# Kernel optimization log

Hardware: AMD Instinct MI355X
Metric: run time of the kernel (lower is better)

## Reference

```python
import jax, jax.numpy as jnp
import numpy as np
from jax import lax

DIM = 256
HEAD_DIM = 64          # v head dim and hedgehog dim
HEAD_DIM_QK = 64       # must equal HEAD_DIM for the module to run
NH = DIM // HEAD_DIM   # 4
EPS = 1e-6


def setup_inputs() -> dict:
    key = jax.random.key(0)
    ks = jax.random.split(key, 12)
    B, C, H, W, D = 1, DIM, 16, 16, 16
    x = jax.random.normal(ks[0], (B, C, H, W, D), dtype=jnp.float32)
    qk_dim = HEAD_DIM_QK * NH
    # 1x1x1 conv weights for q, k (qkv_bias=False)
    Wq = jax.random.normal(ks[1], (qk_dim, C), dtype=jnp.float32) * 0.02
    Wk = jax.random.normal(ks[2], (qk_dim, C), dtype=jnp.float32) * 0.02
    # depthwise 3x3x3 conv for v (groups=dim, bias=True)
    Wv = jax.random.normal(ks[3], (C, 1, 3, 3, 3), dtype=jnp.float32) * 0.1
    bv = jax.random.normal(ks[4], (C,), dtype=jnp.float32) * 0.02
    # HedgeHog linear layers (init is identity/zeros; use near-identity + noise)
    eye = jnp.eye(HEAD_DIM, dtype=jnp.float32)
    Wmq = eye * 0.5 + jax.random.normal(ks[5], (HEAD_DIM, HEAD_DIM), dtype=jnp.float32) * 0.02
    bmq = jnp.zeros((HEAD_DIM,), dtype=jnp.float32)
    Wmk = eye * 0.5 + jax.random.normal(ks[6], (HEAD_DIM, HEAD_DIM), dtype=jnp.float32) * 0.02
    bmk = jnp.zeros((HEAD_DIM,), dtype=jnp.float32)
    Wmv = eye * 0.5 + jax.random.normal(ks[7], (HEAD_DIM, HEAD_DIM), dtype=jnp.float32) * 0.02
    bmv = jnp.zeros((HEAD_DIM,), dtype=jnp.float32)
    return {"x": x, "Wq": Wq, "Wk": Wk, "Wv": Wv, "bv": bv,
            "Wmq": Wmq, "bmq": bmq, "Wmk": Wmk, "bmk": bmk,
            "Wmv": Wmv, "bmv": bmv}


def _hedgehog(z, W, b):
    # z: [B, nh, N, d] -> [B, 2*nh, N, d]; cat along HEAD axis (dim=1) as in torch code
    h = jnp.einsum('bhnd,ed->bhne', z, W) + b
    return jnp.concatenate([jnp.exp(h), jnp.exp(-h)], axis=1)


def reference(x, Wq, Wk, Wv, bv, Wmq, bmq, Wmk, bmk, Wmv, bmv):
    B, C, H, W_, D = x.shape
    N = H * W_ * D
    x2 = x.reshape(B, C, N)
    # 1x1x1 conv projections
    q = jnp.einsum('oc,bcn->bon', Wq, x2)  # [B, qk_dim, N]
    k = jnp.einsum('oc,bcn->bon', Wk, x2)
    # depthwise 3x3x3 conv for v
    v3 = lax.conv_general_dilated(
        x, Wv, window_strides=(1, 1, 1),
        padding=((1, 1), (1, 1), (1, 1)),
        dimension_numbers=('NCDHW', 'OIDHW', 'NCDHW'),
        feature_group_count=C) + bv[None, :, None, None, None]
    v = v3.reshape(B, C, N)
    # split heads, tokens-last -> tokens axis
    q1 = q.reshape(B, NH, HEAD_DIM_QK, N).transpose(0, 1, 3, 2)  # [B,nh,N,dqk]
    k1 = k.reshape(B, NH, HEAD_DIM_QK, N).transpose(0, 1, 3, 2)
    v1 = v.reshape(B, NH, HEAD_DIM, N).transpose(0, 1, 3, 2)     # [B,nh,N,dv]
    qf = _hedgehog(q1, Wmq, bmq)  # [B,2nh,N,dqk]
    kf = _hedgehog(k1, Wmk, bmk)
    vf = _hedgehog(v1, Wmv, bmv)  # [B,2nh,N,dv]
    # quadratic "linear" attention: row-sum normalized QK^T
    qk = jnp.einsum('bhmd,bhnd->bhmn', qf, kf)          # [B,2nh,N,N]
    attn = qk / (jnp.sum(qk, axis=-1, keepdims=True) + EPS)
    out = jnp.einsum('bhmn,bhnd->bhmd', attn, vf)        # [B,2nh,N,dv]
    out = out.transpose(0, 1, 3, 2).reshape(B, 2 * C, H, W_, D)
    return out
```

## Files before the change

### kernel.cpp

```cpp
#include <hip/hip_runtime.h>
#include <math.h>

#define EPS_F 1e-6f

typedef __attribute__((ext_vector_type(8))) short bf16x8;
typedef __attribute__((ext_vector_type(4))) float f32x4;

#define OFF_BV  0
#define OFF_VC  (OFF_BV + 256)
#define OFF_PS  (OFF_VC + 256*4096)
#define OFF_PSV (OFF_PS + 8*64*4096)
#define OFF_SM  (OFF_PSV + 8*64*64)
#define OFF_SV  (OFF_SM + 8*4096)
#define OFF_QF  (OFF_SV + 512)
#define OFF_WQH (OFF_QF + 512*4096)
#define OFF_WQL (OFF_WQH + 32768)
#define OFF_WKH (OFF_WQL + 32768)
#define OFF_WKL (OFF_WKH + 32768)
#define OFF_XTH (OFF_WKL + 32768)
#define OFF_XTL (OFF_XTH + 524288)

__device__ __forceinline__ void split_bf16(float v, unsigned short& h, unsigned short& l) {
    unsigned int b = __float_as_uint(v);
    h = (unsigned short)(b >> 16);
    float fh = __uint_as_float(b & 0xFFFF0000u);
    l = (unsigned short)(__float_as_uint(v - fh) >> 16);
}

__global__ __launch_bounds__(256) void k_combine(
    const float* __restrict__ Wq, const float* __restrict__ Wk,
    const float* __restrict__ Wmq, const float* __restrict__ Wmk,
    const float* __restrict__ Wmv, const float* __restrict__ bmv,
    const float* __restrict__ bv, float* __restrict__ ws)
{
    int row = blockIdx.x;
    int c = threadIdx.x;
    int h = row >> 6, e = row & 63;
    float aq = 0.f, ak = 0.f;
    for (int d = 0; d < 64; ++d) {
        float mq = Wmq[e*64 + d];
        float mk = Wmk[e*64 + d];
        int src = (h*64 + d)*256 + c;
        aq = fmaf(mq, Wq[src], aq);
        ak = fmaf(mk, Wk[src], ak);
    }
    unsigned short hh, ll;
    unsigned short* WQH = (unsigned short*)(ws + OFF_WQH);
    unsigned short* WQL = (unsigned short*)(ws + OFF_WQL);
    unsigned short* WKH = (unsigned short*)(ws + OFF_WKH);
    unsigned short* WKL = (unsigned short*)(ws + OFF_WKL);
    split_bf16(aq, hh, ll); WQH[row*256 + c] = hh; WQL[row*256 + c] = ll;
    split_bf16(ak, hh, ll); WKH[row*256 + c] = hh; WKL[row*256 + c] = ll;
    if (c == 0) {
        float av = 0.f;
        for (int d = 0; d < 64; ++d) av = fmaf(Wmv[e*64 + d], bv[h*64 + d], av);
        ws[OFF_BV + row] = av + bmv[e];
    }
}

__global__ __launch_bounds__(256) void k_xt(
    const float* __restrict__ x, float* __restrict__ ws)
{
    __shared__ float Ts[64][65];
    int tx = blockIdx.x;
    int cy = blockIdx.y;
    int t = threadIdx.x;
    int lr = t >> 6, lc2 = t & 63;
    #pragma unroll
    for (int i = 0; i < 16; ++i) {
        int row = lr*16 + i;
        Ts[row][lc2] = x[(size_t)(cy*64 + row)*4096 + tx*64 + lc2];
    }
    __syncthreads();
    int tok = t >> 2, c16 = (t & 3) * 16;
    unsigned int hw[8], lw[8];
    #pragma unroll
    for (int j = 0; j < 8; ++j) {
        float v0 = Ts[c16 + 2*j][tok], v1 = Ts[c16 + 2*j + 1][tok];
        unsigned int b0 = __float_as_uint(v0), b1 = __float_as_uint(v1);
        hw[j] = (b0 >> 16) | (b1 & 0xFFFF0000u);
        float f0 = __uint_as_float(b0 & 0xFFFF0000u);
        float f1 = __uint_as_float(b1 & 0xFFFF0000u);
        lw[j] = (__float_as_uint(v0 - f0) >> 16) | (__float_as_uint(v1 - f1) & 0xFFFF0000u);
    }
    unsigned short* XH = (unsigned short*)(ws + OFF_XTH);
    unsigned short* XL = (unsigned short*)(ws + OFF_XTL);
    size_t base = (size_t)(tx*64 + tok)*256 + cy*64 + c16;
    uint4 H0 = {hw[0], hw[1], hw[2], hw[3]}, H1 = {hw[4], hw[5], hw[6], hw[7]};
    uint4 L0 = {lw[0], lw[1], lw[2], lw[3]}, L1 = {lw[4], lw[5], lw[6], lw[7]};
    *(uint4*)(XH + base) = H0;  *(uint4*)(XH + base + 8) = H1;
    *(uint4*)(XL + base) = L0;  *(uint4*)(XL + base + 8) = L1;
}

__global__ __launch_bounds__(256) void k_dwconv(
    const float* __restrict__ x, const float* __restrict__ Wv, float* __restrict__ vc)
{
    int c = blockIdx.y;
    int n = blockIdx.x * 256 + threadIdx.x;
    int z = n >> 8, y = (n >> 4) & 15, xx = n & 15;
    const float* xc = x + c * 4096;
    const float* wc = Wv + c * 27;
    float acc = 0.f;
    #pragma unroll
    for (int kz = 0; kz < 3; ++kz) {
        int zz = z + kz - 1;
        if (zz < 0 || zz > 15) continue;
        #pragma unroll
        for (int ky = 0; ky < 3; ++ky) {
            int yy = y + ky - 1;
            if (yy < 0 || yy > 15) continue;
            #pragma unroll
            for (int kx = 0; kx < 3; ++kx) {
                int xv = xx + kx - 1;
                if (xv < 0 || xv > 15) continue;
                acc = fmaf(wc[(kz*3 + ky)*3 + kx], xc[(zz << 8) + (yy << 4) + xv], acc);
            }
        }
    }
    vc[c*4096 + n] = acc;
}

__global__ __launch_bounds__(512, 2) void k_fused(
    const float* __restrict__ bmk, const float* __restrict__ bmq,
    const float* __restrict__ Wmv, float* __restrict__ ws)
{
    __shared__ float smem[16384];
    unsigned short* su = (unsigned short*)smem;

    int t = threadIdx.x;
    int chunk = blockIdx.x;
    int hb = blockIdx.y;
    int n0 = chunk * 64;
    int w = t >> 6, lane = t & 63;
    int kq = w >> 2;
    int mh = w & 1, nh = (w >> 1) & 1;
    int l15 = lane & 15, l4 = lane >> 4;
    bool isQ = (t >= 256);
    int tl = t & 255;
    int lc = tl >> 6, ln = tl & 63;
    int e4 = (tl & 15) * 4;
    int n4 = (tl >> 4) * 4;

    const unsigned short* XH  = (const unsigned short*)(ws + OFF_XTH);
    const unsigned short* XL  = (const unsigned short*)(ws + OFF_XTL);
    const unsigned short* WKHp = (const unsigned short*)(ws + OFF_WKH);
    const unsigned short* WKLp = (const unsigned short*)(ws + OFF_WKL);
    const unsigned short* WQHp = (const unsigned short*)(ws + OFF_WQH);
    const unsigned short* WQLp = (const unsigned short*)(ws + OFF_WQL);

    f32x4 acc[2][2];
    #pragma unroll
    for (int i = 0; i < 2; ++i)
        #pragma unroll
        for (int j = 0; j < 2; ++j) acc[i][j] = (f32x4){0.f, 0.f, 0.f, 0.f};
    float accV[4][4];
    #pragma unroll
    for (int i = 0; i < 4; ++i)
        #pragma unroll
        for (int j = 0; j < 4; ++j) accV[i][j] = 0.f;

    for (int cs = 0; cs < 4; ++cs) {
        int c0 = cs * 64;
        {
            int r = (t >> 3) & 63, s = t & 7;
            unsigned short* d = su + r*64 + (((s ^ (r & 7))) << 3);
            size_t xo = (size_t)(n0 + r)*256 + c0 + s*8;
            size_t wo = (size_t)(hb*64 + r)*256 + c0 + s*8;
            *(uint4*)(d)         = *(const uint4*)(XH + xo);
            *(uint4*)(d + 4096)  = *(const uint4*)(XL + xo);
            *(uint4*)(d + 8192)  = *(const uint4*)(WKHp + wo);
            *(uint4*)(d + 12288) = *(const uint4*)(WKLp + wo);
            *(uint4*)(d + 16384) = *(const uint4*)(WQHp + wo);
            *(uint4*)(d + 20480) = *(const uint4*)(WQLp + wo);
        }
        __syncthreads();
        const unsigned short* Xh = su;
        const unsigned short* Xl = su + 4096;
        const unsigned short* Wh = su + 8192 + kq*8192;
        const unsigned short* Wl = Wh + 4096;
        #pragma unroll
        for (int ks = 0; ks < 2; ++ks) {
            bf16x8 ah[2], al[2], bh_[2], bl_[2];
            #pragma unroll
            for (int mt = 0; mt < 2; ++mt) {
                int ar = mh*32 + mt*16 + l15;
                int off = ar*64 + (((ks*4 + l4) ^ (ar & 7)) << 3);
                ah[mt] = *(const bf16x8*)(Xh + off);
                al[mt] = *(const bf16x8*)(Xl + off);
            }
            #pragma unroll
            for (int nt = 0; nt < 2; ++nt) {
                int br = nh*32 + nt*16 + l15;
                int off = br*64 + (((ks*4 + l4) ^ (br & 7)) << 3);
                bh_[nt] = *(const bf16x8*)(Wh + off);
                bl_[nt] = *(const bf16x8*)(Wl + off);
            }
            #pragma unroll
            for (int mt = 0; mt < 2; ++mt)
                #pragma unroll
                for (int nt = 0; nt < 2; ++nt) {
                    acc[mt][nt] = __builtin_amdgcn_mfma_f32_16x16x32_bf16(ah[mt], bh_[nt], acc[mt][nt], 0, 0, 0);
                    acc[mt][nt] = __builtin_amdgcn_mfma_f32_16x16x32_bf16(al[mt], bh_[nt], acc[mt][nt], 0, 0, 0);
                    acc[mt][nt] = __builtin_amdgcn_mfma_f32_16x16x32_bf16(ah[mt], bl_[nt], acc[mt][nt], 0, 0, 0);
                }
        }
        __syncthreads();
    }

    float (*Xs)[64]  = (float(*)[64])smem;
    float (*Wsh)[68] = (float(*)[68])(smem + 4096);
    if (!isQ) {
        const float* vcb = ws + OFF_VC + (size_t)hb*64*4096;
        #pragma unroll
        for (int i = 0; i < 16; ++i)
            Xs[lc*16 + i][ln] = vcb[(size_t)(lc*16 + i)*4096 + n0 + ln];
        #pragma unroll
        for (int i = 0; i < 16; ++i) { int idx = i*256 + tl; Wsh[idx & 63][idx >> 6] = Wmv[idx]; }
    }
    __syncthreads();

    if (!isQ) {
        #pragma unroll 4
        for (int d = 0; d < 64; ++d) {
            float4 xv4 = *(const float4*)&Xs[d][n4];
            float4 wv4 = *(const float4*)&Wsh[d][e4];
            float xv[4] = {xv4.x, xv4.y, xv4.z, xv4.w};
            float wv[4] = {wv4.x, wv4.y, wv4.z, wv4.w};
            #pragma unroll
            for (int ii = 0; ii < 4; ++ii)
                #pragma unroll
                for (int jj = 0; jj < 4; ++jj)
                    accV[ii][jj] = fmaf(xv[ii], wv[jj], accV[ii][jj]);
        }
    }
    __syncthreads();

    float (*kfp)[64] = (float(*)[64])smem;
    float (*kfm)[64] = (float(*)[64])(smem + 4096);
    float (*vfp)[64] = (float(*)[64])(smem + 8192);
    float (*vfm)[64] = (float(*)[64])(smem + 12288);
    if (!isQ) {
        float bk0 = bmk[nh*32 + l15], bk1 = bmk[nh*32 + 16 + l15];
        #pragma unroll
        for (int mt = 0; mt < 2; ++mt)
            #pragma unroll
            for (int nt = 0; nt < 2; ++nt) {
                float bkv = nt ? bk1 : bk0;
                int feat = nh*32 + nt*16 + l15;
                #pragma unroll
                for (int r = 0; r < 4; ++r) {
                    int tok = mh*32 + mt*16 + l4*4 + r;
                    float v = acc[mt][nt][r] + bkv;
                    kfp[tok][feat] = __expf(v);
                    kfm[tok][feat] = __expf(-v);
                }
            }
        float bvv[4];
        #pragma unroll
        for (int j = 0; j < 4; ++j) bvv[j] = ws[OFF_BV + hb*64 + e4 + j];
        #pragma unroll
        for (int ii = 0; ii < 4; ++ii) {
            float pv[4], mv[4];
            #pragma unroll
            for (int jj = 0; jj < 4; ++jj) {
                float b = accV[ii][jj] + bvv[jj];
                pv[jj] = __expf(b);  mv[jj] = __expf(-b);
            }
            *(float4*)&vfp[n4 + ii][e4] = make_float4(pv[0], pv[1], pv[2], pv[3]);
            *(float4*)&vfm[n4 + ii][e4] = make_float4(mv[0], mv[1], mv[2], mv[3]);
        }
    }
    __syncthreads();

    float aSp[4][4], aSm[4][4], svp[4], svm[4];
    #pragma unroll
    for (int i = 0; i < 4; ++i) {
        svp[i] = 0.f; svm[i] = 0.f;
        #pragma unroll
        for (int j = 0; j < 4; ++j) { aSp[i][j] = 0.f; aSm[i][j] = 0.f; }
    }
    int a4 = e4, f4 = n4;
    int nb = isQ ? 32 : 0;
    #pragma unroll 2
    for (int nn = 0; nn < 32; ++nn) {
        int n = nb + nn;
        float4 kp4 = *(const float4*)&kfp[n][a4];
        float4 km4 = *(const float4*)&kfm[n][a4];
        float4 vp4 = *(const float4*)&vfp[n][f4];
        float4 vm4 = *(const float4*)&vfm[n][f4];
        float kp[4] = {kp4.x, kp4.y, kp4.z, kp4.w};
        float km[4] = {km4.x, km4.y, km4.z, km4.w};
        float vp[4] = {vp4.x, vp4.y, vp4.z, vp4.w};
        float vm[4] = {vm4.x, vm4.y, vm4.z, vm4.w};
        #pragma unroll
        for (int ai = 0; ai < 4; ++ai) {
            svp[ai] += kp[ai];  svm[ai] += km[ai];
            #pragma unroll
            for (int fi = 0; fi < 4; ++fi) {
                aSp[ai][fi] = fmaf(kp[ai], vp[fi], aSp[ai][fi]);
                aSm[ai][fi] = fmaf(km[ai], vm[fi], aSm[ai][fi]);
            }
        }
    }
    __syncthreads();

    if (isQ) {
        #pragma unroll
        for (int i = 0; i < 4; ++i)
            #pragma unroll
            for (int j = 0; j < 4; ++j) {
                smem[(i*4 + j)*256 + tl]      = aSp[i][j];
                smem[(16 + i*4 + j)*256 + tl] = aSm[i][j];
            }
        if (tl < 16) {
            #pragma unroll
            for (int i = 0; i < 4; ++i) {
                smem[8192 + i*16 + tl]      = svp[i];
                smem[8192 + 64 + i*16 + tl] = svm[i];
            }
        }
    }
    __syncthreads();
    if (!isQ) {
        #pragma unroll
        for (int i = 0; i < 4; ++i)
            #pragma unroll
            for (int j = 0; j < 4; ++j) {
                aSp[i][j] += smem[(i*4 + j)*256 + tl];
                aSm[i][j] += smem[(16 + i*4 + j)*256 + tl];
            }
        float* pSp = ws + OFF_PS + (size_t)(hb*64 + chunk)*4096;
        float* pSm = ws + OFF_PS + (size_t)((hb + 4)*64 + chunk)*4096;
        #pragma unroll
        for (int ai = 0; ai < 4; ++ai) {
            *(float4*)&pSp[(a4 + ai)*64 + f4] = make_float4(aSp[ai][0], aSp[ai][1], aSp[ai][2], aSp[ai][3]);
            *(float4*)&pSm[(a4 + ai)*64 + f4] = make_float4(aSm[ai][0], aSm[ai][1], aSm[ai][2], aSm[ai][3]);
        }
        if (tl < 16) {
            #pragma unroll
            for (int i = 0; i < 4; ++i) {
                svp[i] += smem[8192 + i*16 + tl];
                svm[i] += smem[8192 + 64 + i*16 + tl];
            }
            float* pvp = ws + OFF_PSV + (size_t)(hb*64 + chunk)*64;
            float* pvm = ws + OFF_PSV + (size_t)((hb + 4)*64 + chunk)*64;
            *(float4*)&pvp[a4] = make_float4(svp[0], svp[1], svp[2], svp[3]);
            *(float4*)&pvm[a4] = make_float4(svm[0], svm[1], svm[2], svm[3]);
        }
    }
    __syncthreads();

    float (*qTp)[68] = (float(*)[68])smem;
    float (*qTm)[68] = (float(*)[68])(smem + 4352);
    if (isQ) {
        float bq0 = bmq[nh*32 + l15], bq1 = bmq[nh*32 + 16 + l15];
        #pragma unroll
        for (int mt = 0; mt < 2; ++mt)
            #pragma unroll
            for (int nt = 0; nt < 2; ++nt) {
                float bqv = nt ? bq1 : bq0;
                int feat = nh*32 + nt*16 + l15;
                #pragma unroll
                for (int r = 0; r < 4; ++r) {
                    int tok = mh*32 + mt*16 + l4*4 + r;
                    float v = acc[mt][nt][r] + bqv;
                    qTp[feat][tok] = __expf(v);
                    qTm[feat][tok] = __expf(-v);
                }
            }
    }
    __syncthreads();
    float* gq = ws + OFF_QF;
    #pragma unroll
    for (int j = 0; j < 4; ++j) {
        int un = t + 512*j;
        int s = un >> 10;
        int rem = un & 1023;
        int feat = rem >> 4, t4 = (rem & 15) * 4;
        const float* src = (s ? &qTm[feat][t4] : &qTp[feat][t4]);
        float4 v = *(const float4*)src;
        *(float4*)&gq[(size_t)((hb + 4*s)*64 + feat)*4096 + n0 + t4] = v;
    }
}

__global__ __launch_bounds__(256) void k_reduce(float* __restrict__ ws)
{
    int idx = blockIdx.x*256 + threadIdx.x;
    if (idx < 8*4096) {
        int h = idx >> 12, r = idx & 4095;
        float s = 0.f;
        #pragma unroll 16
        for (int c = 0; c < 64; ++c) s += ws[OFF_PS + (size_t)(h*64 + c)*4096 + r];
        ws[OFF_SM + idx] = s;
    } else if (idx < 8*4096 + 512) {
        int j = idx - 8*4096;
        int h = j >> 6, e = j & 63;
        float s = 0.f;
        #pragma unroll 16
        for (int c = 0; c < 64; ++c) s += ws[OFF_PSV + (size_t)(h*64 + c)*64 + e];
        ws[OFF_SV + j] = s;
    }
}

__global__ __launch_bounds__(256, 2) void k_out(
    const float* __restrict__ ws, float* __restrict__ out)
{
    __shared__ float qs[64][64];
    __shared__ float Sms[64][64];
    __shared__ float svs[64];
    int t = threadIdx.x;
    int chunk = blockIdx.x;
    int h = blockIdx.y;
    int n0 = chunk * 64;
    int lc = t >> 6, ln = t & 63;

    const float* gq = ws + OFF_QF + (size_t)h*64*4096;
    #pragma unroll
    for (int i = 0; i < 16; ++i)
        qs[lc*16 + i][ln] = gq[(size_t)(lc*16 + i)*4096 + n0 + ln];
    const float* Smg = ws + OFF_SM + (size_t)h*4096;
    #pragma unroll
    for (int i = 0; i < 16; ++i) { int idx = i*256 + t; Sms[idx >> 6][idx & 63] = Smg[idx]; }
    if (t < 64) svs[t] = ws[OFF_SV + h*64 + t];
    __syncthreads();

    int n4 = (t & 15) * 4;
    int e4 = (t >> 4) * 4;
    float acc[4][4];
    float den[4] = {0.f, 0.f, 0.f, 0.f};
    #pragma unroll
    for (int i = 0; i < 4; ++i)
        #pragma unroll
        for (int j = 0; j < 4; ++j) acc[i][j] = 0.f;
    #pragma unroll 4
    for (int a = 0; a < 64; ++a) {
        float4 qv4 = *(const float4*)&qs[a][n4];
        float4 sm4 = *(const float4*)&Sms[a][e4];
        float qv[4] = {qv4.x, qv4.y, qv4.z, qv4.w};
        float sm[4] = {sm4.x, sm4.y, sm4.z, sm4.w};
        float sva = svs[a];
        #pragma unroll
        for (int nj = 0; nj < 4; ++nj) {
            den[nj] = fmaf(qv[nj], sva, den[nj]);
            #pragma unroll
            for (int ei = 0; ei < 4; ++ei)
                acc[ei][nj] = fmaf(sm[ei], qv[nj], acc[ei][nj]);
        }
    }
    float r[4];
    #pragma unroll
    for (int nj = 0; nj < 4; ++nj) r[nj] = 1.f / (den[nj] + EPS_F);
    #pragma unroll
    for (int ei = 0; ei < 4; ++ei)
        *(float4*)&out[(size_t)(h*64 + e4 + ei)*4096 + n0 + n4] =
            make_float4(acc[ei][0]*r[0], acc[ei][1]*r[1], acc[ei][2]*r[2], acc[ei][3]*r[3]);
}

extern "C" void kernel_launch(void* const* d_in, const int* in_sizes, int n_in,
                              void* d_out, int out_size, void* d_ws, size_t ws_size,
                              hipStream_t stream) {
    const float* x   = (const float*)d_in[0];
    const float* Wq  = (const float*)d_in[1];
    const float* Wk  = (const float*)d_in[2];
    const float* Wv  = (const float*)d_in[3];
    const float* bv  = (const float*)d_in[4];
    const float* Wmq = (const float*)d_in[5];
    const float* bmq = (const float*)d_in[6];
    const float* Wmk = (const float*)d_in[7];
    const float* bmk = (const float*)d_in[8];
    const float* Wmv = (const float*)d_in[9];
    const float* bmv = (const float*)d_in[10];
    float* out = (float*)d_out;
    float* ws  = (float*)d_ws;

    k_combine<<<256, 256, 0, stream>>>(Wq, Wk, Wmq, Wmk, Wmv, bmv, bv, ws);
    k_xt<<<dim3(64, 4), 256, 0, stream>>>(x, ws);
    k_dwconv<<<dim3(16, 256), 256, 0, stream>>>(x, Wv, ws + OFF_VC);
    k_fused<<<dim3(64, 4), 512, 0, stream>>>(bmk, bmq, Wmv, ws);
    k_reduce<<<130, 256, 0, stream>>>(ws);
    k_out<<<dim3(64, 8), 256, 0, stream>>>(ws, out);
}
```

Measured before the change: 133.2 us.

## Merge six kernels into one cooperative persistent kernel with grid syncs

Replaces the six separate launches (weight combine, x transpose/split, depthwise conv, fused projection, reduce, output) with a single cooperative kernel of 256 blocks of 512 threads. The stages are separated by grid.sync() barriers, and each block's work is remapped onto its block index. This removes per-launch overhead and inter-kernel gaps for a small, latency-bound problem. In exchange it adds grid-wide barrier cost, and some stages such as the reduce and output run with fewer or idle threads per block.

```diff
diff --git a/kernel.cpp b/kernel.cpp
--- a/kernel.cpp
+++ b/kernel.cpp
@@ -1,5 +1,8 @@
 #include <hip/hip_runtime.h>
+#include <hip/hip_cooperative_groups.h>
 #include <math.h>
+
+namespace cg = cooperative_groups;
 
 #define EPS_F 1e-6f
 
@@ -27,433 +30,436 @@
     l = (unsigned short)(__float_as_uint(v - fh) >> 16);
 }
 
-__global__ __launch_bounds__(256) void k_combine(
+__global__ __launch_bounds__(512, 2) void k_mega(
+    const float* __restrict__ x,
     const float* __restrict__ Wq, const float* __restrict__ Wk,
-    const float* __restrict__ Wmq, const float* __restrict__ Wmk,
+    const float* __restrict__ Wv, const float* __restrict__ bv,
+    const float* __restrict__ Wmq, const float* __restrict__ bmq,
+    const float* __restrict__ Wmk, const float* __restrict__ bmk,
     const float* __restrict__ Wmv, const float* __restrict__ bmv,
-    const float* __restrict__ bv, float* __restrict__ ws)
-{
-    int row = blockIdx.x;
-    int c = threadIdx.x;
-    int h = row >> 6, e = row & 63;
-    float aq = 0.f, ak = 0.f;
-    for (int d = 0; d < 64; ++d) {
-        float mq = Wmq[e*64 + d];
-        float mk = Wmk[e*64 + d];
-        int src = (h*64 + d)*256 + c;
-        aq = fmaf(mq, Wq[src], aq);
-        ak = fmaf(mk, Wk[src], ak);
-    }
-    unsigned short hh, ll;
-    unsigned short* WQH = (unsigned short*)(ws + OFF_WQH);
-    unsigned short* WQL = (unsigned short*)(ws + OFF_WQL);
-    unsigned short* WKH = (unsigned short*)(ws + OFF_WKH);
-    unsigned short* WKL = (unsigned short*)(ws + OFF_WKL);
-    split_bf16(aq, hh, ll); WQH[row*256 + c] = hh; WQL[row*256 + c] = ll;
-    split_bf16(ak, hh, ll); WKH[row*256 + c] = hh; WKL[row*256 + c] = ll;
-    if (c == 0) {
-        float av = 0.f;
-        for (int d = 0; d < 64; ++d) av = fmaf(Wmv[e*64 + d], bv[h*64 + d], av);
-        ws[OFF_BV + row] = av + bmv[e];
-    }
-}
-
-__global__ __launch_bounds__(256) void k_xt(
-    const float* __restrict__ x, float* __restrict__ ws)
-{
-    __shared__ float Ts[64][65];
-    int tx = blockIdx.x;
-    int cy = blockIdx.y;
-    int t = threadIdx.x;
-    int lr = t >> 6, lc2 = t & 63;
-    #pragma unroll
-    for (int i = 0; i < 16; ++i) {
-        int row = lr*16 + i;
-        Ts[row][lc2] = x[(size_t)(cy*64 + row)*4096 + tx*64 + lc2];
-    }
-    __syncthreads();
-    int tok = t >> 2, c16 = (t & 3) * 16;
-    unsigned int hw[8], lw[8];
-    #pragma unroll
-    for (int j = 0; j < 8; ++j) {
-        float v0 = Ts[c16 + 2*j][tok], v1 = Ts[c16 + 2*j + 1][tok];
-        unsigned int b0 = __float_as_uint(v0), b1 = __float_as_uint(v1);
-        hw[j] = (b0 >> 16) | (b1 & 0xFFFF0000u);
-        float f0 = __uint_as_float(b0 & 0xFFFF0000u);
-        float f1 = __uint_as_float(b1 & 0xFFFF0000u);
-        lw[j] = (__float_as_uint(v0 - f0) >> 16) | (__float_as_uint(v1 - f1) & 0xFFFF0000u);
-    }
-    unsigned short* XH = (unsigned short*)(ws + OFF_XTH);
-    unsigned short* XL = (unsigned short*)(ws + OFF_XTL);
-    size_t base = (size_t)(tx*64 + tok)*256 + cy*64 + c16;
-    uint4 H0 = {hw[0], hw[1], hw[2], hw[3]}, H1 = {hw[4], hw[5], hw[6], hw[7]};
-    uint4 L0 = {lw[0], lw[1], lw[2], lw[3]}, L1 = {lw[4], lw[5], lw[6], lw[7]};
-    *(uint4*)(XH + base) = H0;  *(uint4*)(XH + base + 8) = H1;
-    *(uint4*)(XL + base) = L0;  *(uint4*)(XL + base + 8) = L1;
-}
-
-__global__ __launch_bounds__(256) void k_dwconv(
-    const float* __restrict__ x, const float* __restrict__ Wv, float* __restrict__ vc)
-{
-    int c = blockIdx.y;
-    int n = blockIdx.x * 256 + threadIdx.x;
-    int z = n >> 8, y = (n >> 4) & 15, xx = n & 15;
-    const float* xc = x + c * 4096;
-    const float* wc = Wv + c * 27;
-    float acc = 0.f;
-    #pragma unroll
-    for (int kz = 0; kz < 3; ++kz) {
-        int zz = z + kz - 1;
-        if (zz < 0 || zz > 15) continue;
-        #pragma unroll
-        for (int ky = 0; ky < 3; ++ky) {
-            int yy = y + ky - 1;
-            if (yy < 0 || yy > 15) continue;
-            #pragma unroll
-            for (int kx = 0; kx < 3; ++kx) {
-                int xv = xx + kx - 1;
-                if (xv < 0 || xv > 15) continue;
-                acc = fmaf(wc[(kz*3 + ky)*3 + kx], xc[(zz << 8) + (yy << 4) + xv], acc);
-            }
-        }
-    }
-    vc[c*4096 + n] = acc;
-}
-
-__global__ __launch_bounds__(512, 2) void k_fused(
-    const float* __restrict__ bmk, const float* __restrict__ bmq,
-    const float* __restrict__ Wmv, float* __restrict__ ws)
+    float* __restrict__ ws, float* __restrict__ out)
 {
     __shared__ float smem[16384];
-    unsigned short* su = (unsigned short*)smem;
-
+    cg::grid_group grid = cg::this_grid();
+    int b = blockIdx.x;
     int t = threadIdx.x;
-    int chunk = blockIdx.x;
-    int hb = blockIdx.y;
-    int n0 = chunk * 64;
-    int w = t >> 6, lane = t & 63;
-    int kq = w >> 2;
-    int mh = w & 1, nh = (w >> 1) & 1;
-    int l15 = lane & 15, l4 = lane >> 4;
-    bool isQ = (t >= 256);
-    int tl = t & 255;
-    int lc = tl >> 6, ln = tl & 63;
-    int e4 = (tl & 15) * 4;
-    int n4 = (tl >> 4) * 4;
-
-    const unsigned short* XH  = (const unsigned short*)(ws + OFF_XTH);
-    const unsigned short* XL  = (const unsigned short*)(ws + OFF_XTL);
-    const unsigned short* WKHp = (const unsigned short*)(ws + OFF_WKH);
-    const unsigned short* WKLp = (const unsigned short*)(ws + OFF_WKL);
-    const unsigned short* WQHp = (const unsigned short*)(ws + OFF_WQH);
-    const unsigned short* WQLp = (const unsigned short*)(ws + OFF_WQL);
-
-    f32x4 acc[2][2];
-    #pragma unroll
-    for (int i = 0; i < 2; ++i)
-        #pragma unroll
-        for (int j = 0; j < 2; ++j) acc[i][j] = (f32x4){0.f, 0.f, 0.f, 0.f};
-    float accV[4][4];
-    #pragma unroll
-    for (int i = 0; i < 4; ++i)
-        #pragma unroll
-        for (int j = 0; j < 4; ++j) accV[i][j] = 0.f;
-
-    for (int cs = 0; cs < 4; ++cs) {
-        int c0 = cs * 64;
-        {
-            int r = (t >> 3) & 63, s = t & 7;
-            unsigned short* d = su + r*64 + (((s ^ (r & 7))) << 3);
-            size_t xo = (size_t)(n0 + r)*256 + c0 + s*8;
-            size_t wo = (size_t)(hb*64 + r)*256 + c0 + s*8;
-            *(uint4*)(d)         = *(const uint4*)(XH + xo);
-            *(uint4*)(d + 4096)  = *(const uint4*)(XL + xo);
-            *(uint4*)(d + 8192)  = *(const uint4*)(WKHp + wo);
-            *(uint4*)(d + 12288) = *(const uint4*)(WKLp + wo);
-            *(uint4*)(d + 16384) = *(const uint4*)(WQHp + wo);
-            *(uint4*)(d + 20480) = *(const uint4*)(WQLp + wo);
-        }
-        __syncthreads();
-        const unsigned short* Xh = su;
-        const unsigned short* Xl = su + 4096;
-        const unsigned short* Wh = su + 8192 + kq*8192;
-        const unsigned short* Wl = Wh + 4096;
-        #pragma unroll
-        for (int ks = 0; ks < 2; ++ks) {
-            bf16x8 ah[2], al[2], bh_[2], bl_[2];
-            #pragma unroll
-            for (int mt = 0; mt < 2; ++mt) {
-                int ar = mh*32 + mt*16 + l15;
-                int off = ar*64 + (((ks*4 + l4) ^ (ar & 7)) << 3);
-                ah[mt] = *(const bf16x8*)(Xh + off);
-                al[mt] = *(const bf16x8*)(Xl + off);
-            }
-            #pragma unroll
-            for (int nt = 0; nt < 2; ++nt) {
-                int br = nh*32 + nt*16 + l15;
-                int off = br*64 + (((ks*4 + l4) ^ (br & 7)) << 3);
-                bh_[nt] = *(const bf16x8*)(Wh + off);
-                bl_[nt] = *(const bf16x8*)(Wl + off);
-            }
+
+    if (t < 256) {
+        int row = b, c = t;
+        int h = row >> 6, e = row & 63;
+        float aq = 0.f, ak = 0.f;
+        for (int d = 0; d < 64; ++d) {
+            float mq = Wmq[e*64 + d];
+            float mk = Wmk[e*64 + d];
+            int src = (h*64 + d)*256 + c;
+            aq = fmaf(mq, Wq[src], aq);
+            ak = fmaf(mk, Wk[src], ak);
+        }
+        unsigned short hh, ll;
+        unsigned short* WQH = (unsigned short*)(ws + OFF_WQH);
+        unsigned short* WQL = (unsigned short*)(ws + OFF_WQL);
+        unsigned short* WKH = (unsigned short*)(ws + OFF_WKH);
+        unsigned short* WKL = (unsigned short*)(ws + OFF_WKL);
+        split_bf16(aq, hh, ll); WQH[row*256 + c] = hh; WQL[row*256 + c] = ll;
+        split_bf16(ak, hh, ll); WKH[row*256 + c] = hh; WKL[row*256 + c] = ll;
+        if (c == 0) {
+            float av = 0.f;
+            for (int d = 0; d < 64; ++d) av = fmaf(Wmv[e*64 + d], bv[h*64 + d], av);
+            ws[OFF_BV + row] = av + bmv[e];
+        }
+    }
+    {
+        float (*Ts)[65] = (float(*)[65])smem;
+        int tx = b & 63, cy = b >> 6;
+        int lr = t >> 6, lc2 = t & 63;
+        #pragma unroll
+        for (int i = 0; i < 8; ++i) {
+            int row = lr*8 + i;
+            Ts[row][lc2] = x[(size_t)(cy*64 + row)*4096 + tx*64 + lc2];
+        }
+        __syncthreads();
+        int tok = t >> 3, c8 = (t & 7) * 8;
+        unsigned int hw[4], lw[4];
+        #pragma unroll
+        for (int j = 0; j < 4; ++j) {
+            float v0 = Ts[c8 + 2*j][tok], v1 = Ts[c8 + 2*j + 1][tok];
+            unsigned int b0 = __float_as_uint(v0), b1 = __float_as_uint(v1);
+            hw[j] = (b0 >> 16) | (b1 & 0xFFFF0000u);
+            float f0 = __uint_as_float(b0 & 0xFFFF0000u);
+            float f1 = __uint_as_float(b1 & 0xFFFF0000u);
+            lw[j] = (__float_as_uint(v0 - f0) >> 16) | (__float_as_uint(v1 - f1) & 0xFFFF0000u);
+        }
+        unsigned short* XH = (unsigned short*)(ws + OFF_XTH);
+        unsigned short* XL = (unsigned short*)(ws + OFF_XTL);
+        size_t base = (size_t)(tx*64 + tok)*256 + cy*64 + c8;
+        uint4 H = {hw[0], hw[1], hw[2], hw[3]};
+        uint4 L = {lw[0], lw[1], lw[2], lw[3]};
+        *(uint4*)(XH + base) = H;
+        *(uint4*)(XL + base) = L;
+        __syncthreads();
+    }
+    {
+        int c = b;
+        const float* xc = x + c * 4096;
+        const float* wc = Wv + c * 27;
+        #pragma unroll
+        for (int i = 0; i < 8; ++i) {
+            int n = t + 512*i;
+            int z = n >> 8, y = (n >> 4) & 15, xx = n & 15;
+            float acc = 0.f;
+            #pragma unroll
+            for (int kz = 0; kz < 3; ++kz) {
+                int zz = z + kz - 1;
+                if (zz < 0 || zz > 15) continue;
+                #pragma unroll
+                for (int ky = 0; ky < 3; ++ky) {
+                    int yy = y + ky - 1;
+                    if (yy < 0 || yy > 15) continue;
+                    #pragma unroll
+                    for (int kx = 0; kx < 3; ++kx) {
+                        int xv = xx + kx - 1;
+                        if (xv < 0 || xv > 15) continue;
+                        acc = fmaf(wc[(kz*3 + ky)*3 + kx], xc[(zz << 8) + (yy << 4) + xv], acc);
+                    }
+                }
+            }
+            ws[OFF_VC + (size_t)c*4096 + n] = acc;
+        }
+    }
+    grid.sync();
+
+    {
+        unsigned short* su = (unsigned short*)smem;
+        int chunk = b & 63;
+        int hb = b >> 6;
+        int n0 = chunk * 64;
+        int w = t >> 6, lane = t & 63;
+        int kq = w >> 2;
+        int mh = w & 1, nh = (w >> 1) & 1;
+        int l15 = lane & 15, l4 = lane >> 4;
+        bool isQ = (t >= 256);
+        int tl = t & 255;
+        int lc = tl >> 6, ln = tl & 63;
+        int e4 = (tl & 15) * 4;
+        int n4 = (tl >> 4) * 4;
+
+        const unsigned short* XH  = (const unsigned short*)(ws + OFF_XTH);
+        const unsigned short* XL  = (const unsigned short*)(ws + OFF_XTL);
+        const unsigned short* WKHp = (const unsigned short*)(ws + OFF_WKH);
+        const unsigned short* WKLp = (const unsigned short*)(ws + OFF_WKL);
+        const unsigned short* WQHp = (const unsigned short*)(ws + OFF_WQH);
+        const unsigned short* WQLp = (const unsigned short*)(ws + OFF_WQL);
+
+        f32x4 acc[2][2];
+        #pragma unroll
+        for (int i = 0; i < 2; ++i)
+            #pragma unroll
+            for (int j = 0; j < 2; ++j) acc[i][j] = (f32x4){0.f, 0.f, 0.f, 0.f};
+        float accV[4][4];
+        #pragma unroll
+        for (int i = 0; i < 4; ++i)
+            #pragma unroll
+            for (int j = 0; j < 4; ++j) accV[i][j] = 0.f;
+
+        for (int cs = 0; cs < 4; ++cs) {
+            int c0 = cs * 64;
+            {
+                int r = (t >> 3) & 63, s = t & 7;
+                unsigned short* d = su + r*64 + (((s ^ (r & 7))) << 3);
+                size_t xo = (size_t)(n0 + r)*256 + c0 + s*8;
+                size_t wo = (size_t)(hb*64 + r)*256 + c0 + s*8;
+                *(uint4*)(d)         = *(const uint4*)(XH + xo);
+                *(uint4*)(d + 4096)  = *(const uint4*)(XL + xo);
+                *(uint4*)(d + 8192)  = *(const uint4*)(WKHp + wo);
+                *(uint4*)(d + 12288) = *(const uint4*)(WKLp + wo);
+                *(uint4*)(d + 16384) = *(const uint4*)(WQHp + wo);
+                *(uint4*)(d + 20480) = *(const uint4*)(WQLp + wo);
+            }
+            __syncthreads();
+            const unsigned short* Xh = su;
+            const unsigned short* Xl = su + 4096;
+            const unsigned short* Wh = su + 8192 + kq*8192;
+            const unsigned short* Wl = Wh + 4096;
+            #pragma unroll
+            for (int ks = 0; ks < 2; ++ks) {
+                bf16x8 ah[2], al[2], bh_[2], bl_[2];
+                #pragma unroll
+                for (int mt = 0; mt < 2; ++mt) {
+                    int ar = mh*32 + mt*16 + l15;
+                    int off = ar*64 + (((ks*4 + l4) ^ (ar & 7)) << 3);
+                    ah[mt] = *(const bf16x8*)(Xh + off);
+                    al[mt] = *(const bf16x8*)(Xl + off);
+                }
+                #pragma unroll
+                for (int nt = 0; nt < 2; ++nt) {
+                    int br = nh*32 + nt*16 + l15;
+                    int off = br*64 + (((ks*4 + l4) ^ (br & 7)) << 3);
+                    bh_[nt] = *(const bf16x8*)(Wh + off);
+                    bl_[nt] = *(const bf16x8*)(Wl + off);
+                }
+                #pragma unroll
+                for (int mt = 0; mt < 2; ++mt)
+                    #pragma unroll
+                    for (int nt = 0; nt < 2; ++nt) {
+                        acc[mt][nt] = __builtin_amdgcn_mfma_f32_16x16x32_bf16(ah[mt], bh_[nt], acc[mt][nt], 0, 0, 0);
+                        acc[mt][nt] = __builtin_amdgcn_mfma_f32_16x16x32_bf16(al[mt], bh_[nt], acc[mt][nt], 0, 0, 0);
+                        acc[mt][nt] = __builtin_amdgcn_mfma_f32_16x16x32_bf16(ah[mt], bl_[nt], acc[mt][nt], 0, 0, 0);
+                    }
+            }
+            __syncthreads();
+        }
+
+        float (*Xs)[64]  = (float(*)[64])smem;
+        float (*Wsh)[68] = (float(*)[68])(smem + 4096);
+        if (!isQ) {
+            const float* vcb = ws + OFF_VC + (size_t)hb*64*4096;
+            #pragma unroll
+            for (int i = 0; i < 16; ++i)
+                Xs[lc*16 + i][ln] = vcb[(size_t)(lc*16 + i)*4096 + n0 + ln];
+            #pragma unroll
+            for (int i = 0; i < 16; ++i) { int idx = i*256 + tl; Wsh[idx & 63][idx >> 6] = Wmv[idx]; }
+        }
+        __syncthreads();
+
+        if (!isQ) {
+            #pragma unroll 4
+            for (int d = 0; d < 64; ++d) {
+                float4 xv4 = *(const float4*)&Xs[d][n4];
+                float4 wv4 = *(const float4*)&Wsh[d][e4];
+                float xv[4] = {xv4.x, xv4.y, xv4.z, xv4.w};
+                float wv[4] = {wv4.x, wv4.y, wv4.z, wv4.w};
+                #pragma unroll
+                for (int ii = 0; ii < 4; ++ii)
+                    #pragma unroll
+                    for (int jj = 0; jj < 4; ++jj)
+                        accV[ii][jj] = fmaf(xv[ii], wv[jj], accV[ii][jj]);
+            }
+        }
+        __syncthreads();
+
+        float (*kfp)[64] = (float(*)[64])smem;
+        float (*kfm)[64] = (float(*)[64])(smem + 4096);
+        float (*vfp)[64] = (float(*)[64])(smem + 8192);
+        float (*vfm)[64] = (float(*)[64])(smem + 12288);
+        if (!isQ) {
+            float bk0 = bmk[nh*32 + l15], bk1 = bmk[nh*32 + 16 + l15];
             #pragma unroll
             for (int mt = 0; mt < 2; ++mt)
                 #pragma unroll
                 for (int nt = 0; nt < 2; ++nt) {
-                    acc[mt][nt] = __builtin_amdgcn_mfma_f32_16x16x32_bf16(ah[mt], bh_[nt], acc[mt][nt], 0, 0, 0);
-                    acc[mt][nt] = __builtin_amdgcn_mfma_f32_16x16x32_bf16(al[mt], bh_[nt], acc[mt][nt], 0, 0, 0);
-                    acc[mt][nt] = __builtin_amdgcn_mfma_f32_16x16x32_bf16(ah[mt], bl_[nt], acc[mt][nt], 0, 0, 0);
-                }
-        }
-        __syncthreads();
-    }
-
-    float (*Xs)[64]  = (float(*)[64])smem;
-    float (*Wsh)[68] = (float(*)[68])(smem + 4096);
-    if (!isQ) {
-        const float* vcb = ws + OFF_VC + (size_t)hb*64*4096;
+                    float bkv = nt ? bk1 : bk0;
+                    int feat = nh*32 + nt*16 + l15;
+                    #pragma unroll
+                    for (int r = 0; r < 4; ++r) {
+                        int tok = mh*32 + mt*16 + l4*4 + r;
+                        float v = acc[mt][nt][r] + bkv;
+                        kfp[tok][feat] = __expf(v);
+                        kfm[tok][feat] = __expf(-v);
+                    }
+                }
+            float bvv[4];
+            #pragma unroll
+            for (int j = 0; j < 4; ++j) bvv[j] = ws[OFF_BV + hb*64 + e4 + j];
+            #pragma unroll
+            for (int ii = 0; ii < 4; ++ii) {
+                float pv[4], mv[4];
+                #pragma unroll
+                for (int jj = 0; jj < 4; ++jj) {
+                    float bb = accV[ii][jj] + bvv[jj];
+                    pv[jj] = __expf(bb);  mv[jj] = __expf(-bb);
+                }
+                *(float4*)&vfp[n4 + ii][e4] = make_float4(pv[0], pv[1], pv[2], pv[3]);
+                *(float4*)&vfm[n4 + ii][e4] = make_float4(mv[0], mv[1], mv[2], mv[3]);
+            }
+        }
+        __syncthreads();
+
+        float aSp[4][4], aSm[4][4], svp[4], svm[4];
+        #pragma unroll
+        for (int i = 0; i < 4; ++i) {
+            svp[i] = 0.f; svm[i] = 0.f;
+            #pragma unroll
+            for (int j = 0; j < 4; ++j) { aSp[i][j] = 0.f; aSm[i][j] = 0.f; }
+        }
+        int a4 = e4, f4 = n4;
+        int nb = isQ ? 32 : 0;
+        #pragma unroll 2
+        for (int nn = 0; nn < 32; ++nn) {
+            int n = nb + nn;
+            float4 kp4 = *(const float4*)&kfp[n][a4];
+            float4 km4 = *(const float4*)&kfm[n][a4];
+            float4 vp4 = *(const float4*)&vfp[n][f4];
+            float4 vm4 = *(const float4*)&vfm[n][f4];
+            float kp[4] = {kp4.x, kp4.y, kp4.z, kp4.w};
+            float km[4] = {km4.x, km4.y, km4.z, km4.w};
+            float vp[4] = {vp4.x, vp4.y, vp4.z, vp4.w};
+            float vm[4] = {vm4.x, vm4.y, vm4.z, vm4.w};
+            #pragma unroll
+            for (int ai = 0; ai < 4; ++ai) {
+                svp[ai] += kp[ai];  svm[ai] += km[ai];
+                #pragma unroll
+                for (int fi = 0; fi < 4; ++fi) {
+                    aSp[ai][fi] = fmaf(kp[ai], vp[fi], aSp[ai][fi]);
+                    aSm[ai][fi] = fmaf(km[ai], vm[fi], aSm[ai][fi]);
+                }
+            }
+        }
+        __syncthreads();
+
+        if (isQ) {
+            #pragma unroll
+            for (int i = 0; i < 4; ++i)
+                #pragma unroll
+                for (int j = 0; j < 4; ++j) {
+                    smem[(i*4 + j)*256 + tl]      = aSp[i][j];
+                    smem[(16 + i*4 + j)*256 + tl] = aSm[i][j];
+                }
+            if (tl < 16) {
+                #pragma unroll
+                for (int i = 0; i < 4; ++i) {
+                    smem[8192 + i*16 + tl]      = svp[i];
+                    smem[8192 + 64 + i*16 + tl] = svm[i];
+                }
+            }
+        }
+        __syncthreads();
+        if (!isQ) {
+            #pragma unroll
+            for (int i = 0; i < 4; ++i)
+                #pragma unroll
+                for (int j = 0; j < 4; ++j) {
+                    aSp[i][j] += smem[(i*4 + j)*256 + tl];
+                    aSm[i][j] += smem[(16 + i*4 + j)*256 + tl];
+                }
+            float* pSp = ws + OFF_PS + (size_t)(hb*64 + chunk)*4096;
+            float* pSm = ws + OFF_PS + (size_t)((hb + 4)*64 + chunk)*4096;
+            #pragma unroll
+            for (int ai = 0; ai < 4; ++ai) {
+                *(float4*)&pSp[(a4 + ai)*64 + f4] = make_float4(aSp[ai][0], aSp[ai][1], aSp[ai][2], aSp[ai][3]);
+                *(float4*)&pSm[(a4 + ai)*64 + f4] = make_float4(aSm[ai][0], aSm[ai][1], aSm[ai][2], aSm[ai][3]);
+            }
+            if (tl < 16) {
+                #pragma unroll
+                for (int i = 0; i < 4; ++i) {
+                    svp[i] += smem[8192 + i*16 + tl];
+                    svm[i] += smem[8192 + 64 + i*16 + tl];
+                }
+                float* pvp = ws + OFF_PSV + (size_t)(hb*64 + chunk)*64;
+                float* pvm = ws + OFF_PSV + (size_t)((hb + 4)*64 + chunk)*64;
+                *(float4*)&pvp[a4] = make_float4(svp[0], svp[1], svp[2], svp[3]);
+                *(float4*)&pvm[a4] = make_float4(svm[0], svm[1], svm[2], svm[3]);
+            }
+        }
+        __syncthreads();
+
+        float (*qTp)[68] = (float(*)[68])smem;
+        float (*qTm)[68] = (float(*)[68])(smem + 4352);
+        if (isQ) {
+            float bq0 = bmq[nh*32 + l15], bq1 = bmq[nh*32 + 16 + l15];
+            #pragma unroll
+            for (int mt = 0; mt < 2; ++mt)
+                #pragma unroll
+                for (int nt = 0; nt < 2; ++nt) {
+                    float bqv = nt ? bq1 : bq0;
+                    int feat = nh*32 + nt*16 + l15;
+                    #pragma unroll
+                    for (int r = 0; r < 4; ++r) {
+                        int tok = mh*32 + mt*16 + l4*4 + r;
+                        float v = acc[mt][nt][r] + bqv;
+                        qTp[feat][tok] = __expf(v);
+                        qTm[feat][tok] = __expf(-v);
+                    }
+                }
+        }
+        __syncthreads();
+        float* gq = ws + OFF_QF;
+        #pragma unroll
+        for (int j = 0; j < 4; ++j) {
+            int un = t + 512*j;
+            int s = un >> 10;
+            int rem = un & 1023;
+            int feat = rem >> 4, t4 = (rem & 15) * 4;
+            const float* src = (s ? &qTm[feat][t4] : &qTp[feat][t4]);
+            float4 v = *(const float4*)src;
+            *(float4*)&gq[(size_t)((hb + 4*s)*64 + feat)*4096 + n0 + t4] = v;
+        }
+    }
+    grid.sync();
+
+    {
+        int idx = b*512 + t;
+        if (idx < 8*4096) {
+            int h = idx >> 12, r = idx & 4095;
+            float s = 0.f;
+            #pragma unroll 16
+            for (int c = 0; c < 64; ++c) s += ws[OFF_PS + (size_t)(h*64 + c)*4096 + r];
+            ws[OFF_SM + idx] = s;
+        } else if (idx < 8*4096 + 512) {
+            int j = idx - 8*4096;
+            int h = j >> 6, e = j & 63;
+            float s = 0.f;
+            #pragma unroll 16
+            for (int c = 0; c < 64; ++c) s += ws[OFF_PSV + (size_t)(h*64 + c)*64 + e];
+            ws[OFF_SV + j] = s;
+        }
+    }
+    grid.sync();
+
+    {
+        float* qs0 = smem;
+        float* qs1 = smem + 4096;
+        float (*Sms)[64] = (float(*)[64])(smem + 8192);
+        float* svs = smem + 12288;
+        int h = b >> 5;
+        int uh = t >> 8, th = t & 255;
+        int chunk = (b & 31) * 2 + uh;
+        int n0 = chunk * 64;
+        float* qs = uh ? qs1 : qs0;
+        int lc = th >> 6, ln = th & 63;
+
+        const float* gq = ws + OFF_QF + (size_t)h*64*4096;
         #pragma unroll
         for (int i = 0; i < 16; ++i)
-            Xs[lc*16 + i][ln] = vcb[(size_t)(lc*16 + i)*4096 + n0 + ln];
-        #pragma unroll
-        for (int i = 0; i < 16; ++i) { int idx = i*256 + tl; Wsh[idx & 63][idx >> 6] = Wmv[idx]; }
-    }
-    __syncthreads();
-
-    if (!isQ) {
+            qs[(lc*16 + i)*64 + ln] = gq[(size_t)(lc*16 + i)*4096 + n0 + ln];
+        if (uh == 0) {
+            const float* Smg = ws + OFF_SM + (size_t)h*4096;
+            #pragma unroll
+            for (int i = 0; i < 16; ++i) { int idx = i*256 + th; Sms[idx >> 6][idx & 63] = Smg[idx]; }
+        }
+        if (t < 64) svs[t] = ws[OFF_SV + h*64 + t];
+        __syncthreads();
+
+        int n4 = (th & 15) * 4;
+        int e4 = (th >> 4) * 4;
+        float acc[4][4];
+        float den[4] = {0.f, 0.f, 0.f, 0.f};
+        #pragma unroll
+        for (int i = 0; i < 4; ++i)
+            #pragma unroll
+            for (int j = 0; j < 4; ++j) acc[i][j] = 0.f;
         #pragma unroll 4
-        for (int d = 0; d < 64; ++d) {
-            float4 xv4 = *(const float4*)&Xs[d][n4];
-            float4 wv4 = *(const float4*)&Wsh[d][e4];
-            float xv[4] = {xv4.x, xv4.y, xv4.z, xv4.w};
-            float wv[4] = {wv4.x, wv4.y, wv4.z, wv4.w};
-            #pragma unroll
-            for (int ii = 0; ii < 4; ++ii)
-                #pragma unroll
-                for (int jj = 0; jj < 4; ++jj)
-                    accV[ii][jj] = fmaf(xv[ii], wv[jj], accV[ii][jj]);
-        }
-    }
-    __syncthreads();
-
-    float (*kfp)[64] = (float(*)[64])smem;
-    float (*kfm)[64] = (float(*)[64])(smem + 4096);
-    float (*vfp)[64] = (float(*)[64])(smem + 8192);
-    float (*vfm)[64] = (float(*)[64])(smem + 12288);
-    if (!isQ) {
-        float bk0 = bmk[nh*32 + l15], bk1 = bmk[nh*32 + 16 + l15];
-        #pragma unroll
-        for (int mt = 0; mt < 2; ++mt)
-            #pragma unroll
-            for (int nt = 0; nt < 2; ++nt) {
-                float bkv = nt ? bk1 : bk0;
-                int feat = nh*32 + nt*16 + l15;
-                #pragma unroll
-                for (int r = 0; r < 4; ++r) {
-                    int tok = mh*32 + mt*16 + l4*4 + r;
-                    float v = acc[mt][nt][r] + bkv;
-                    kfp[tok][feat] = __expf(v);
-                    kfm[tok][feat] = __expf(-v);
-                }
-            }
-        float bvv[4];
-        #pragma unroll
-        for (int j = 0; j < 4; ++j) bvv[j] = ws[OFF_BV + hb*64 + e4 + j];
-        #pragma unroll
-        for (int ii = 0; ii < 4; ++ii) {
-            float pv[4], mv[4];
-            #pragma unroll
-            for (int jj = 0; jj < 4; ++jj) {
-                float b = accV[ii][jj] + bvv[jj];
-                pv[jj] = __expf(b);  mv[jj] = __expf(-b);
-            }
-            *(float4*)&vfp[n4 + ii][e4] = make_float4(pv[0], pv[1], pv[2], pv[3]);
-            *(float4*)&vfm[n4 + ii][e4] = make_float4(mv[0], mv[1], mv[2], mv[3]);
-        }
-    }
-    __syncthreads();
-
-    float aSp[4][4], aSm[4][4], svp[4], svm[4];
-    #pragma unroll
-    for (int i = 0; i < 4; ++i) {
-        svp[i] = 0.f; svm[i] = 0.f;
-        #pragma unroll
-        for (int j = 0; j < 4; ++j) { aSp[i][j] = 0.f; aSm[i][j] = 0.f; }
-    }
-    int a4 = e4, f4 = n4;
-    int nb = isQ ? 32 : 0;
-    #pragma unroll 2
-    for (int nn = 0; nn < 32; ++nn) {
-        int n = nb + nn;
-        float4 kp4 = *(const float4*)&kfp[n][a4];
-        float4 km4 = *(const float4*)&kfm[n][a4];
-        float4 vp4 = *(const float4*)&vfp[n][f4];
-        float4 vm4 = *(const float4*)&vfm[n][f4];
-        float kp[4] = {kp4.x, kp4.y, kp4.z, kp4.w};
-        float km[4] = {km4.x, km4.y, km4.z, km4.w};
-        float vp[4] = {vp4.x, vp4.y, vp4.z, vp4.w};
-        float vm[4] = {vm4.x, vm4.y, vm4.z, vm4.w};
-        #pragma unroll
-        for (int ai = 0; ai < 4; ++ai) {
-            svp[ai] += kp[ai];  svm[ai] += km[ai];
-            #pragma unroll
-            for (int fi = 0; fi < 4; ++fi) {
-                aSp[ai][fi] = fmaf(kp[ai], vp[fi], aSp[ai][fi]);
-                aSm[ai][fi] = fmaf(km[ai], vm[fi], aSm[ai][fi]);
-            }
-        }
-    }
-    __syncthreads();
-
-    if (isQ) {
-        #pragma unroll
-        for (int i = 0; i < 4; ++i)
-            #pragma unroll
-            for (int j = 0; j < 4; ++j) {
-                smem[(i*4 + j)*256 + tl]      = aSp[i][j];
-                smem[(16 + i*4 + j)*256 + tl] = aSm[i][j];
-            }
-        if (tl < 16) {
-            #pragma unroll
-            for (int i = 0; i < 4; ++i) {
-                smem[8192 + i*16 + tl]      = svp[i];
-                smem[8192 + 64 + i*16 + tl] = svm[i];
-            }
-        }
-    }
-    __syncthreads();
-    if (!isQ) {
-        #pragma unroll
-        for (int i = 0; i < 4; ++i)
-            #pragma unroll
-            for (int j = 0; j < 4; ++j) {
-                aSp[i][j] += smem[(i*4 + j)*256 + tl];
-                aSm[i][j] += smem[(16 + i*4 + j)*256 + tl];
-            }
-        float* pSp = ws + OFF_PS + (size_t)(hb*64 + chunk)*4096;
-        float* pSm = ws + OFF_PS + (size_t)((hb + 4)*64 + chunk)*4096;
-        #pragma unroll
-        for (int ai = 0; ai < 4; ++ai) {
-            *(float4*)&pSp[(a4 + ai)*64 + f4] = make_float4(aSp[ai][0], aSp[ai][1], aSp[ai][2], aSp[ai][3]);
-            *(float4*)&pSm[(a4 + ai)*64 + f4] = make_float4(aSm[ai][0], aSm[ai][1], aSm[ai][2], aSm[ai][3]);
-        }
-        if (tl < 16) {
-            #pragma unroll
-            for (int i = 0; i < 4; ++i) {
-                svp[i] += smem[8192 + i*16 + tl];
-                svm[i] += smem[8192 + 64 + i*16 + tl];
-            }
-            float* pvp = ws + OFF_PSV + (size_t)(hb*64 + chunk)*64;
-            float* pvm = ws + OFF_PSV + (size_t)((hb + 4)*64 + chunk)*64;
-            *(float4*)&pvp[a4] = make_float4(svp[0], svp[1], svp[2], svp[3]);
-            *(float4*)&pvm[a4] = make_float4(svm[0], svm[1], svm[2], svm[3]);
-        }
-    }
-    __syncthreads();
-
-    float (*qTp)[68] = (float(*)[68])smem;
-    float (*qTm)[68] = (float(*)[68])(smem + 4352);
-    if (isQ) {
-        float bq0 = bmq[nh*32 + l15], bq1 = bmq[nh*32 + 16 + l15];
-        #pragma unroll
-        for (int mt = 0; mt < 2; ++mt)
-            #pragma unroll
-            for (int nt = 0; nt < 2; ++nt) {
-                float bqv = nt ? bq1 : bq0;
-                int feat = nh*32 + nt*16 + l15;
-                #pragma unroll
-                for (int r = 0; r < 4; ++r) {
-                    int tok = mh*32 + mt*16 + l4*4 + r;
-                    float v = acc[mt][nt][r] + bqv;
-                    qTp[feat][tok] = __expf(v);
-                    qTm[feat][tok] = __expf(-v);
-                }
-            }
-    }
-    __syncthreads();
-    float* gq = ws + OFF_QF;
-    #pragma unroll
-    for (int j = 0; j < 4; ++j) {
-        int un = t + 512*j;
-        int s = un >> 10;
-        int rem = un & 1023;
-        int feat = rem >> 4, t4 = (rem & 15) * 4;
-        const float* src = (s ? &qTm[feat][t4] : &qTp[feat][t4]);
-        float4 v = *(const float4*)src;
-        *(float4*)&gq[(size_t)((hb + 4*s)*64 + feat)*4096 + n0 + t4] = v;
-    }
-}
-
-__global__ __launch_bounds__(256) void k_reduce(float* __restrict__ ws)
-{
-    int idx = blockIdx.x*256 + threadIdx.x;
-    if (idx < 8*4096) {
-        int h = idx >> 12, r = idx & 4095;
-        float s = 0.f;
-        #pragma unroll 16
-        for (int c = 0; c < 64; ++c) s += ws[OFF_PS + (size_t)(h*64 + c)*4096 + r];
-        ws[OFF_SM + idx] = s;
-    } else if (idx < 8*4096 + 512) {
-        int j = idx - 8*4096;
-        int h = j >> 6, e = j & 63;
-        float s = 0.f;
-        #pragma unroll 16
-        for (int c = 0; c < 64; ++c) s += ws[OFF_PSV + (size_t)(h*64 + c)*64 + e];
-        ws[OFF_SV + j] = s;
-    }
-}
-
-__global__ __launch_bounds__(256, 2) void k_out(
-    const float* __restrict__ ws, float* __restrict__ out)
-{
-    __shared__ float qs[64][64];
-    __shared__ float Sms[64][64];
-    __shared__ float svs[64];
-    int t = threadIdx.x;
-    int chunk = blockIdx.x;
-    int h = blockIdx.y;
-    int n0 = chunk * 64;
-    int lc = t >> 6, ln = t & 63;
-
-    const float* gq = ws + OFF_QF + (size_t)h*64*4096;
-    #pragma unroll
-    for (int i = 0; i < 16; ++i)
-        qs[lc*16 + i][ln] = gq[(size_t)(lc*16 + i)*4096 + n0 + ln];
-    const float* Smg = ws + OFF_SM + (size_t)h*4096;
-    #pragma unroll
-    for (int i = 0; i < 16; ++i) { int idx = i*256 + t; Sms[idx >> 6][idx & 63] = Smg[idx]; }
-    if (t < 64) svs[t] = ws[OFF_SV + h*64 + t];
-    __syncthreads();
-
-    int n4 = (t & 15) * 4;
-    int e4 = (t >> 4) * 4;
-    float acc[4][4];
-    float den[4] = {0.f, 0.f, 0.f, 0.f};
-    #pragma unroll
-    for (int i = 0; i < 4; ++i)
-        #pragma unroll
-        for (int j = 0; j < 4; ++j) acc[i][j] = 0.f;
-    #pragma unroll 4
-    for (int a = 0; a < 64; ++a) {
-        float4 qv4 = *(const float4*)&qs[a][n4];
-        float4 sm4 = *(const float4*)&Sms[a][e4];
-        float qv[4] = {qv4.x, qv4.y, qv4.z, qv4.w};
-        float sm[4] = {sm4.x, sm4.y, sm4.z, sm4.w};
-        float sva = svs[a];
-        #pragma unroll
-        for (int nj = 0; nj < 4; ++nj) {
-            den[nj] = fmaf(qv[nj], sva, den[nj]);
-            #pragma unroll
-            for (int ei = 0; ei < 4; ++ei)
-                acc[ei][nj] = fmaf(sm[ei], qv[nj], acc[ei][nj]);
-        }
-    }
-    float r[4];
-    #pragma unroll
-    for (int nj = 0; nj < 4; ++nj) r[nj] = 1.f / (den[nj] + EPS_F);
-    #pragma unroll
-    for (int ei = 0; ei < 4; ++ei)
-        *(float4*)&out[(size_t)(h*64 + e4 + ei)*4096 + n0 + n4] =
-            make_float4(acc[ei][0]*r[0], acc[ei][1]*r[1], acc[ei][2]*r[2], acc[ei][3]*r[3]);
+        for (int a = 0; a < 64; ++a) {
+            float4 qv4 = *(const float4*)&qs[a*64 + n4];
+            float4 sm4 = *(const float4*)&Sms[a][e4];
+            float qv[4] = {qv4.x, qv4.y, qv4.z, qv4.w};
+            float sm[4] = {sm4.x, sm4.y, sm4.z, sm4.w};
+            float sva = svs[a];
+            #pragma unroll
+            for (int nj = 0; nj < 4; ++nj) {
+                den[nj] = fmaf(qv[nj], sva, den[nj]);
+                #pragma unroll
+                for (int ei = 0; ei < 4; ++ei)
+                    acc[ei][nj] = fmaf(sm[ei], qv[nj], acc[ei][nj]);
+            }
+        }
+        float r[4];
+        #pragma unroll
+        for (int nj = 0; nj < 4; ++nj) r[nj] = 1.f / (den[nj] + EPS_F);
+        #pragma unroll
+        for (int ei = 0; ei < 4; ++ei)
+            *(float4*)&out[(size_t)(h*64 + e4 + ei)*4096 + n0 + n4] =
+                make_float4(acc[ei][0]*r[0], acc[ei][1]*r[1], acc[ei][2]*r[2], acc[ei][3]*r[3]);
+    }
 }
 
 extern "C" void kernel_launch(void* const* d_in, const int* in_sizes, int n_in,
@@ -473,10 +479,10 @@
     float* out = (float*)d_out;
     float* ws  = (float*)d_ws;
 
-    k_combine<<<256, 256, 0, stream>>>(Wq, Wk, Wmq, Wmk, Wmv, bmv, bv, ws);
-    k_xt<<<dim3(64, 4), 256, 0, stream>>>(x, ws);
-    k_dwconv<<<dim3(16, 256), 256, 0, stream>>>(x, Wv, ws + OFF_VC);
-    k_fused<<<dim3(64, 4), 512, 0, stream>>>(bmk, bmq, Wmv, ws);
-    k_reduce<<<130, 256, 0, stream>>>(ws);
-    k_out<<<dim3(64, 8), 256, 0, stream>>>(ws, out);
+    void* kargs[] = {
+        (void*)&x, (void*)&Wq, (void*)&Wk, (void*)&Wv, (void*)&bv,
+        (void*)&Wmq, (void*)&bmq, (void*)&Wmk, (void*)&bmk,
+        (void*)&Wmv, (void*)&bmv, (void*)&ws, (void*)&out
+    };
+    hipLaunchCooperativeKernel((void*)k_mega, dim3(256), dim3(512), kargs, 0, stream);
 }
```

Measured after the change: 249.5 us. 87.4% more time.
